# Kernel optimization log

Hardware: AMD Instinct MI355X
Metric: run time of the kernel (lower is better)

The kernel has to match this reference:

```python
import jax, jax.numpy as jnp
import numpy as np

# pywt Wavelet('db4') filter bank (8 taps)
_DEC_LO = np.array([-0.010597401785069032, 0.032883011666982945, 0.030841381835986965,
                    -0.18703481171888114, -0.02798376941698385, 0.6308807679295904,
                    0.7148465705525415, 0.23037781330885523], dtype=np.float32)
_REC_LO = _DEC_LO[::-1].copy()
_DEC_HI = (np.array([(-1.0) ** (k + 1) for k in range(8)], dtype=np.float32) * _REC_LO)
_REC_HI = _DEC_HI[::-1].copy()
_FLEN = 8
_LEVEL = 3


def _corr(x, filt, stride):
    # x: (N, L); cross-correlation with `filt`, VALID, given stride -> (N, Lout)
    k = jnp.asarray(filt.copy())[None, None, :].astype(x.dtype)
    y = jax.lax.conv_general_dilated(x[:, None, :], k, (stride,), 'VALID',
                                     dimension_numbers=('NCH', 'OIH', 'NCH'))
    return y[:, 0, :]


def _dwt(x):
    # pywt dwt, mode='symmetric': pad F-1 each side, full convolution, keep odd phase
    p = _FLEN - 1
    ext = jnp.pad(x, ((0, 0), (p, p)), mode='symmetric')[:, 1:]
    cA = _corr(ext, _DEC_LO[::-1], 2)  # conv == corr with flipped filter
    cD = _corr(ext, _DEC_HI[::-1], 2)
    return cA, cD


def _idwt(a, d):
    # pywt idwt: upsample by 2 (values at even idx), full conv, trim F-2 each side
    n = a.shape[-1]

    def up(c):
        # upsampled (2n-1) with 1 zero of padding on each side -> length 2n+1
        u = jnp.zeros((c.shape[0], 2 * n + 1), c.dtype)
        return u.at[:, 1::2].set(c)

    return _corr(up(a), _REC_LO[::-1], 1) + _corr(up(d), _REC_HI[::-1], 1)


def _waverec(a, details):
    # details ordered coarsest -> finest (as pywt waverec consumes them)
    for d in details:
        if a.shape[-1] == d.shape[-1] + 1:
            a = a[:, :-1]
        a = _idwt(a, d)
    return a


def setup_inputs() -> dict:
    key = jax.random.key(0)
    x = jax.random.normal(key, (32, 64, 16384), dtype=jnp.float32)
    return {"x": x}


def reference(x):
    B, F, L = x.shape
    x2 = x.reshape(B * F, L)

    # wavedec: repeatedly split the approximation
    a = x2
    details = []  # finest first
    for _ in range(_LEVEL):
        a, d = _dwt(a)
        details.append(d)
    details = details[::-1]  # coarsest -> finest, matching waverec order

    low = _waverec(a, [jnp.zeros_like(d) for d in details])
    high = _waverec(jnp.zeros_like(a), details)

    low = low[:, :L].reshape(B, F, L)
    high = high[:, :L].reshape(B, F, L)
    return (low, high)
```

## Files before the change

kernel.cpp:

```cpp
#include <hip/hip_runtime.h>

namespace {
constexpr int kL0      = 16384;
constexpr int kN1      = 8195;
constexpr int kN2      = 4101;
constexpr int kTS      = 2048;
constexpr int kTilesPerRow = kL0 / kTS;
constexpr int kThreads = 256;

constexpr int SX  = 2138;
constexpr int SA1 = 1066;
constexpr int SA2 = 530;
constexpr int SA3 = 262;

constexpr float RLc[8] = {
     0.23037781330885523f,  0.7148465705525415f,   0.6308807679295904f,
    -0.02798376941698385f, -0.18703481171888114f,  0.030841381835986965f,
     0.032883011666982945f, -0.010597401785069032f };

struct WT { float w[8][7]; };
constexpr WT make_w() {
    WT W{};
    for (int r = 0; r < 8; ++r) {
        const int r2 = r >> 1, pi = r & 1;
        for (int u = 0; u < 4; ++u) {
            const float cu = RLc[6 + pi - 2 * u];
            const int k = r2 + u, k2 = k >> 1, pk = k & 1;
            for (int s = 0; s < 4; ++s) {
                const float cs = RLc[6 + pk - 2 * s];
                const int j = k2 + s, j2 = j >> 1, pj = j & 1;
                for (int t = 0; t < 4; ++t)
                    W.w[r][j2 + t] += cu * cs * RLc[6 + pj - 2 * t];
            }
        }
    }
    return W;
}

__device__ constexpr float RL[8] = {
     0.23037781330885523f,  0.7148465705525415f,   0.6308807679295904f,
    -0.02798376941698385f, -0.18703481171888114f,  0.030841381835986965f,
     0.032883011666982945f, -0.010597401785069032f };
__device__ constexpr WT W = make_w();
}

__device__ __forceinline__ int reflect(int g, int N) {
    if (g < 0)  g = -1 - g;
    if (g >= N) g = 2 * N - 1 - g;
    return g;
}

__device__ __forceinline__ float tap8(const float* __restrict__ p) {
    const float2* q = reinterpret_cast<const float2*>(p);
    const float2 q0 = q[0], q1 = q[1], q2 = q[2], q3 = q[3];
    float s = q0.x * RL[0];
    s = fmaf(q0.y, RL[1], s); s = fmaf(q1.x, RL[2], s); s = fmaf(q1.y, RL[3], s);
    s = fmaf(q2.x, RL[4], s); s = fmaf(q2.y, RL[5], s); s = fmaf(q3.x, RL[6], s);
    s = fmaf(q3.y, RL[7], s);
    return s;
}

__global__ void __launch_bounds__(kThreads, 8)
wavelet_tiled(const float* __restrict__ x, float* __restrict__ out, int rows) {
    __shared__ float sx [SX];
    __shared__ float sa1[SA1];
    __shared__ float sa2[SA2];
    __shared__ float sa3[SA3];

    const int tid  = threadIdx.x;
    const int row  = blockIdx.x / kTilesPerRow;
    const int tile = blockIdx.x % kTilesPerRow;
    const int O  = tile * kTS;
    const int X0 = O - 42;
    const int A0 = (O >> 1) - 18;
    const int B0 = (O >> 2) - 6;
    const float* __restrict__ xr = x + (size_t)row * kL0;

    const int t0  = (tile == 0) ? 42 : 2;
    const int thi = (tile == kTilesPerRow - 1) ? 2090 : SX;
    const int Nv  = (thi - t0) >> 2;
    for (int v = tid; v < Nv; v += kThreads) {
        const float4 val = *reinterpret_cast<const float4*>(xr + X0 + t0 + 4 * v);
        float2* dst = reinterpret_cast<float2*>(&sx[t0 + 4 * v]);
        dst[0] = make_float2(val.x, val.y);
        dst[1] = make_float2(val.z, val.w);
    }
    for (int t = tid; t < SX; t += kThreads)
        if (t < t0 || t >= t0 + 4 * Nv)
            sx[t] = xr[reflect(X0 + t, kL0)];
    __syncthreads();

    for (int m = tid; m < SA1; m += kThreads) {
        const int ng = reflect(A0 + m, kN1);
        sa1[m] = tap8(&sx[2 * (ng - A0)]);
    }
    __syncthreads();

    for (int m = tid; m < SA2; m += kThreads) {
        const int ng = reflect(B0 + m, kN2);
        sa2[m] = tap8(&sa1[2 * (ng - B0)]);
    }
    __syncthreads();

    for (int m = tid; m < SA3; m += kThreads)
        sa3[m] = tap8(&sa2[2 * m]);
    __syncthreads();

    float a[7];
    #pragma unroll
    for (int m = 0; m < 7; ++m) a[m] = sa3[tid + m];

    float lo[8];
    #pragma unroll
    for (int r = 0; r < 8; ++r) {
        float s = a[0] * W.w[r][0];
        #pragma unroll
        for (int m = 1; m < 7; ++m) s = fmaf(a[m], W.w[r][m], s);
        lo[r] = s;
    }

    const float4* xr4 = reinterpret_cast<const float4*>(xr + O + 8 * tid);
    const float4 xv0 = xr4[0], xv1 = xr4[1];
    float* __restrict__ lowp  = out + (size_t)row * kL0 + O + 8 * tid;
    float* __restrict__ highp = lowp + (size_t)rows * kL0;
    reinterpret_cast<float4*>(lowp)[0]  = make_float4(lo[0], lo[1], lo[2], lo[3]);
    reinterpret_cast<float4*>(lowp)[1]  = make_float4(lo[4], lo[5], lo[6], lo[7]);
    reinterpret_cast<float4*>(highp)[0] = make_float4(xv0.x - lo[0], xv0.y - lo[1],
                                                      xv0.z - lo[2], xv0.w - lo[3]);
    reinterpret_cast<float4*>(highp)[1] = make_float4(xv1.x - lo[4], xv1.y - lo[5],
                                                      xv1.z - lo[6], xv1.w - lo[7]);
}

extern "C" void kernel_launch(void* const* d_in, const int* in_sizes, int n_in,
                              void* d_out, int out_size, void* d_ws, size_t ws_size,
                              hipStream_t stream) {
    (void)n_in; (void)d_ws; (void)ws_size; (void)out_size;
    const float* x = (const float*)d_in[0];
    float* out = (float*)d_out;
    const int rows = in_sizes[0] / kL0;
    const int blocks = rows * kTilesPerRow;
    hipLaunchKernelGGL(wavelet_tiled, dim3(blocks), dim3(kThreads), 0, stream,
                       x, out, rows);
}
```

Before: 101.9 us.

## Process whole rows per block with async global-to-LDS prefetch of next tile

Result: slower. 116.5 us (+14.3%).

```diff
diff --git a/kernel.cpp b/kernel.cpp
--- a/kernel.cpp
+++ b/kernel.cpp
@@ -1,14 +1,12 @@
 #include <hip/hip_runtime.h>
 
 namespace {
-constexpr int kL0      = 16384;
-constexpr int kN1      = 8195;
-constexpr int kN2      = 4101;
-constexpr int kTS      = 2048;
-constexpr int kTilesPerRow = kL0 / kTS;
+constexpr int kL0 = 16384;
+constexpr int kN1 = 8195;
+constexpr int kN2 = 4101;
 constexpr int kThreads = 256;
 
-constexpr int SX  = 2138;
+constexpr int SXF = 2144;
 constexpr int SA1 = 1066;
 constexpr int SA2 = 530;
 constexpr int SA3 = 262;
@@ -50,7 +48,7 @@
     return g;
 }
 
-__device__ __forceinline__ float tap8(const float* __restrict__ p) {
+__device__ __forceinline__ float tap8f2(const float* __restrict__ p) {
     const float2* q = reinterpret_cast<const float2*>(p);
     const float2 q0 = q[0], q1 = q[1], q2 = q[2], q3 = q[3];
     float s = q0.x * RL[0];
@@ -60,75 +58,110 @@
     return s;
 }
 
+__device__ __forceinline__ void tbar() {
+    asm volatile("s_waitcnt vmcnt(0) lgkmcnt(0)" ::: "memory");
+    __builtin_amdgcn_s_barrier();
+    asm volatile("" ::: "memory");
+}
+__device__ __forceinline__ void pbar() {
+    asm volatile("s_waitcnt lgkmcnt(0)" ::: "memory");
+    __builtin_amdgcn_s_barrier();
+    asm volatile("" ::: "memory");
+}
+
+typedef __attribute__((address_space(1))) const void gvoid_t;
+typedef __attribute__((address_space(3))) void lvoid_t;
+
 __global__ void __launch_bounds__(kThreads, 8)
-wavelet_tiled(const float* __restrict__ x, float* __restrict__ out, int rows) {
-    __shared__ float sx [SX];
-    __shared__ float sa1[SA1];
-    __shared__ float sa2[SA2];
-    __shared__ float sa3[SA3];
+wavelet_pipe(const float* __restrict__ x, float* __restrict__ out, int rows) {
+    __shared__ __align__(16) float sx [SXF];
+    __shared__ __align__(16) float sa1[SA1 + 2];
+    __shared__ __align__(16) float sa2[SA2 + 2];
+    __shared__ __align__(16) float sa3[SA3 + 2];
 
-    const int tid  = threadIdx.x;
-    const int row  = blockIdx.x / kTilesPerRow;
-    const int tile = blockIdx.x % kTilesPerRow;
-    const int O  = tile * kTS;
-    const int X0 = O - 42;
-    const int A0 = (O >> 1) - 18;
-    const int B0 = (O >> 2) - 6;
-    const float* __restrict__ xr = x + (size_t)row * kL0;
+    const int tid = threadIdx.x;
+    const int row = blockIdx.x;
+    const float* __restrict__ xg = x + (size_t)row * kL0;
 
-    const int t0  = (tile == 0) ? 42 : 2;
-    const int thi = (tile == kTilesPerRow - 1) ? 2090 : SX;
-    const int Nv  = (thi - t0) >> 2;
-    for (int v = tid; v < Nv; v += kThreads) {
-        const float4 val = *reinterpret_cast<const float4*>(xr + X0 + t0 + 4 * v);
-        float2* dst = reinterpret_cast<float2*>(&sx[t0 + 4 * v]);
-        dst[0] = make_float2(val.x, val.y);
-        dst[1] = make_float2(val.z, val.w);
+    auto stage = [&](int tt) {
+        const int XB = (tt << 11) - 44;
+        if (tt != 0 && tt != 7) {
+            if (tid < 2) sx[2 + tid] = xg[XB + 2 + tid];
+            const int wv = tid >> 6, lane = tid & 63;
+            for (int c = wv; c <= 8; c += 4) {
+                const int fo = 4 + (c << 8) + (lane << 2);
+                if (c < 8 || lane < 22)
+                    __builtin_amdgcn_global_load_lds((gvoid_t*)(xg + XB + fo),
+                                                     (lvoid_t*)(&sx[fo]), 16, 0, 0);
+            }
+        } else {
+            const int t0  = (tt == 0) ? 44 : 4;
+            const int thi = (tt == 0) ? 2140 : 2092;
+            const int Nv  = (thi - t0) >> 2;
+            for (int v = tid; v < Nv; v += kThreads) {
+                const float4 val = *reinterpret_cast<const float4*>(xg + XB + t0 + 4 * v);
+                sx[t0 + 4 * v]     = val.x; sx[t0 + 4 * v + 1] = val.y;
+                sx[t0 + 4 * v + 2] = val.z; sx[t0 + 4 * v + 3] = val.w;
+            }
+            for (int t = 2 + tid; t < 2140; t += kThreads)
+                if (t < t0 || t >= thi)
+                    sx[t] = xg[reflect(XB + t, kL0)];
+        }
+    };
+
+    stage(0);
+
+    for (int t = 0; t < 8; ++t) {
+        const int O  = t << 11;
+        const int A0 = (O >> 1) - 18;
+        const int B0 = (O >> 2) - 6;
+
+        tbar();
+
+        for (int m = tid; m < SA1; m += kThreads) {
+            const int g  = A0 + m;
+            const int mh = (g >= 0 && g < kN1) ? m : (reflect(g, kN1) - A0);
+            sa1[m] = tap8f2(&sx[2 * mh + 2]);
+        }
+        pbar();
+
+        if (t < 7) stage(t + 1);
+
+        for (int m = tid; m < SA2; m += kThreads) {
+            const int g = B0 + m;
+            const int j = (g >= 0 && g < kN2) ? m : (reflect(g, kN2) - B0);
+            sa2[m] = tap8f2(&sa1[2 * j]);
+        }
+        pbar();
+
+        for (int m = tid; m < SA3; m += kThreads)
+            sa3[m] = tap8f2(&sa2[2 * m]);
+        pbar();
+
+        {
+            const float4* xr4 = reinterpret_cast<const float4*>(xg + O + 8 * tid);
+            const float4 xv0 = xr4[0], xv1 = xr4[1];
+            float a[7];
+            #pragma unroll
+            for (int m = 0; m < 7; ++m) a[m] = sa3[tid + m];
+            float lo[8];
+            #pragma unroll
+            for (int r = 0; r < 8; ++r) {
+                float s = a[0] * W.w[r][0];
+                #pragma unroll
+                for (int m = 1; m < 7; ++m) s = fmaf(a[m], W.w[r][m], s);
+                lo[r] = s;
+            }
+            float* __restrict__ lowp  = out + (size_t)row * kL0 + O + 8 * tid;
+            float* __restrict__ highp = lowp + (size_t)rows * kL0;
+            reinterpret_cast<float4*>(lowp)[0]  = make_float4(lo[0], lo[1], lo[2], lo[3]);
+            reinterpret_cast<float4*>(lowp)[1]  = make_float4(lo[4], lo[5], lo[6], lo[7]);
+            reinterpret_cast<float4*>(highp)[0] = make_float4(xv0.x - lo[0], xv0.y - lo[1],
+                                                              xv0.z - lo[2], xv0.w - lo[3]);
+            reinterpret_cast<float4*>(highp)[1] = make_float4(xv1.x - lo[4], xv1.y - lo[5],
+                                                              xv1.z - lo[6], xv1.w - lo[7]);
+        }
     }
-    for (int t = tid; t < SX; t += kThreads)
-        if (t < t0 || t >= t0 + 4 * Nv)
-            sx[t] = xr[reflect(X0 + t, kL0)];
-    __syncthreads();
-
-    for (int m = tid; m < SA1; m += kThreads) {
-        const int ng = reflect(A0 + m, kN1);
-        sa1[m] = tap8(&sx[2 * (ng - A0)]);
-    }
-    __syncthreads();
-
-    for (int m = tid; m < SA2; m += kThreads) {
-        const int ng = reflect(B0 + m, kN2);
-        sa2[m] = tap8(&sa1[2 * (ng - B0)]);
-    }
-    __syncthreads();
-
-    for (int m = tid; m < SA3; m += kThreads)
-        sa3[m] = tap8(&sa2[2 * m]);
-    __syncthreads();
-
-    float a[7];
-    #pragma unroll
-    for (int m = 0; m < 7; ++m) a[m] = sa3[tid + m];
-
-    float lo[8];
-    #pragma unroll
-    for (int r = 0; r < 8; ++r) {
-        float s = a[0] * W.w[r][0];
-        #pragma unroll
-        for (int m = 1; m < 7; ++m) s = fmaf(a[m], W.w[r][m], s);
-        lo[r] = s;
-    }
-
-    const float4* xr4 = reinterpret_cast<const float4*>(xr + O + 8 * tid);
-    const float4 xv0 = xr4[0], xv1 = xr4[1];
-    float* __restrict__ lowp  = out + (size_t)row * kL0 + O + 8 * tid;
-    float* __restrict__ highp = lowp + (size_t)rows * kL0;
-    reinterpret_cast<float4*>(lowp)[0]  = make_float4(lo[0], lo[1], lo[2], lo[3]);
-    reinterpret_cast<float4*>(lowp)[1]  = make_float4(lo[4], lo[5], lo[6], lo[7]);
-    reinterpret_cast<float4*>(highp)[0] = make_float4(xv0.x - lo[0], xv0.y - lo[1],
-                                                      xv0.z - lo[2], xv0.w - lo[3]);
-    reinterpret_cast<float4*>(highp)[1] = make_float4(xv1.x - lo[4], xv1.y - lo[5],
-                                                      xv1.z - lo[6], xv1.w - lo[7]);
 }
 
 extern "C" void kernel_launch(void* const* d_in, const int* in_sizes, int n_in,
@@ -138,7 +171,6 @@
     const float* x = (const float*)d_in[0];
     float* out = (float*)d_out;
     const int rows = in_sizes[0] / kL0;
-    const int blocks = rows * kTilesPerRow;
-    hipLaunchKernelGGL(wavelet_tiled, dim3(blocks), dim3(kThreads), 0, stream,
+    hipLaunchKernelGGL(wavelet_pipe, dim3(rows), dim3(kThreads), 0, stream,
                        x, out, rows);
 }
```
